# Optimization experiments

Measured on AMD Instinct MI355X. Metric: run time of the kernel, lower is better.

The kernel has to match this reference:

```python
import jax, jax.numpy as jnp
import numpy as np

S = 64            # rendered_size
CLASS_NUM = 14    # dataset.enc_len
NEG_SLOPE = 0.01
EPS = 1e-5


def _conv(x, w, stride, pad):
    return jax.lax.conv_general_dilated(
        x, w, (stride, stride), [(pad, pad), (pad, pad)],
        dimension_numbers=("NCHW", "OIHW", "NCHW"))


def _bn(x, gamma, beta):
    # BatchNorm2d in training mode: biased batch stats over (N,H,W)
    m = jnp.mean(x, axis=(0, 2, 3), keepdims=True)
    v = jnp.var(x, axis=(0, 2, 3), keepdims=True)
    xn = (x - m) * jax.lax.rsqrt(v + EPS)
    return xn * gamma.reshape(1, -1, 1, 1) + beta.reshape(1, -1, 1, 1)


def _lrelu(x):
    return jnp.where(x >= 0, x, NEG_SLOPE * x)


def _render(elements):
    # elements: (B, N, class_num+4)
    rects = elements[:, :, -4:]
    cls = elements[:, :, :-4]                       # (B, N, C)
    x = rects[:, :, 0][:, :, None, None] * S        # (B, N, 1, 1)
    y = rects[:, :, 1][:, :, None, None] * S
    w = rects[:, :, 2][:, :, None, None] * S
    h = rects[:, :, 3][:, :, None, None] * S
    x0, x1 = x - 0.5 * w, x + 0.5 * w
    y0, y1 = y - 0.5 * h, y + 0.5 * h
    cx = jnp.arange(S, dtype=elements.dtype)[None, None, None, :]  # varies along W
    cy = jnp.arange(S, dtype=elements.dtype)[None, None, :, None]  # varies along H
    k = lambda c, cr: jnp.maximum(1.0 - jnp.abs(c - cr), 0.0)
    b0 = lambda c, cr: jnp.clip(c - cr, 0.0, 1.0)
    b1 = lambda cr, c: jnp.clip(cr - c, 0.0, 1.0)
    by = b0(cy, y0) * b1(y1, cy)                    # (B, N, S, S)
    bx = b0(cx, x0) * b1(x1, cx)
    l0 = k(cx, x0) * by
    l1 = k(cx, x1) * by
    l2 = k(cy, y0) * bx
    l3 = k(cy, y1) * bx
    rendered = jnp.maximum(jnp.maximum(l0, l1), jnp.maximum(l2, l3))  # (B,N,S,S)
    # sum over elements of class one-hot * rendered -> (B, C, S, S)
    return jnp.einsum("bnc,bnhw->bchw", cls, rendered)


def setup_inputs() -> dict:
    key = jax.random.key(0)
    ks = jax.random.split(key, 8)
    B, N = 64, 46
    inp = {
        "input_data": jax.random.uniform(ks[0], (B, N, CLASS_NUM + 4), dtype=jnp.float32),
        "input_length": jax.random.randint(ks[1], (B,), 0, N, dtype=jnp.int32),
        # cnn convs (bias=False) + BN affine params
        "w1": jax.random.normal(ks[2], (64, CLASS_NUM, 5, 5), jnp.float32) * 0.05,
        "g1": jnp.ones((64,), jnp.float32), "b1": jnp.zeros((64,), jnp.float32),
        "w2": jax.random.normal(ks[3], (128, 64, 5, 5), jnp.float32) * 0.03,
        "g2": jnp.ones((128,), jnp.float32), "b2": jnp.zeros((128,), jnp.float32),
        "w3": jax.random.normal(ks[4], (256, 128, 5, 5), jnp.float32) * 0.02,
        "g3": jnp.ones((256,), jnp.float32), "b3": jnp.zeros((256,), jnp.float32),
        # classifier: conv k=8 (bias=False) + BN + 1x1 conv (bias=True)
        "w4": jax.random.normal(ks[5], (1024, 256, 8, 8), jnp.float32) * 0.01,
        "g4": jnp.ones((1024,), jnp.float32), "b4": jnp.zeros((1024,), jnp.float32),
        "w5": jax.random.normal(ks[6], (1, 1024, 1, 1), jnp.float32) * 0.03,
        "b5": jnp.zeros((1,), jnp.float32),
    }
    return inp


def reference(input_data, input_length, w1, g1, b1, w2, g2, b2,
              w3, g3, b3, w4, g4, b4, w5, b5):
    rendered = _render(input_data)                       # (B, C, 64, 64)
    h = _lrelu(_bn(_conv(rendered, w1, 2, 2), g1, b1))   # (B, 64, 32, 32)
    h = _lrelu(_bn(_conv(h, w2, 2, 2), g2, b2))          # (B, 128, 16, 16)
    h = _lrelu(_bn(_conv(h, w3, 2, 2), g3, b3))          # (B, 256, 8, 8)
    h = _lrelu(_bn(_conv(h, w4, 1, 0), g4, b4))          # (B, 1024, 1, 1)
    out = _conv(h, w5, 1, 0) + b5.reshape(1, -1, 1, 1)   # (B, 1, 1, 1)
    return out.squeeze()                                 # (B,)
```

## Files before the change

kernel.cpp:

```cpp
#include <hip/hip_runtime.h>
#include <hip/hip_bf16.h>

#define NEG 0.01f
#define EPS 1e-5f

typedef __attribute__((ext_vector_type(8))) short short8;
typedef __attribute__((ext_vector_type(4))) float floatx4;

__device__ inline unsigned short f2bf(float f) {
    __hip_bfloat16 h = __float2bfloat16(f);
    union { __hip_bfloat16 h; unsigned short u; } cv; cv.h = h;
    return cv.u;
}

__global__ __launch_bounds__(256) void render_kernel(const float* __restrict__ in,
                                                     unsigned short* __restrict__ out) {
    int b = blockIdx.x >> 4;
    int chunk = blockIdx.x & 15;
    __shared__ float r0[46], r1[46], r2[46], r3[46];
    __shared__ float cls_s[46 * 14];
    int tid = threadIdx.x;
    if (tid < 46) {
        const float* p = in + ((size_t)b * 46 + tid) * 18 + 14;
        float x = p[0] * 64.f, y = p[1] * 64.f, w = p[2] * 64.f, h = p[3] * 64.f;
        r0[tid] = x - 0.5f * w; r1[tid] = x + 0.5f * w;
        r2[tid] = y - 0.5f * h; r3[tid] = y + 0.5f * h;
    }
    for (int idx = tid; idx < 46 * 14; idx += 256) {
        int n = idx / 14, c = idx % 14;
        cls_s[idx] = in[((size_t)b * 46 + n) * 18 + c];
    }
    __syncthreads();
    if (tid < 33) {
        int j = chunk * 33 + tid;
        if (j < 528) {
            int y, x;
            if (j < 136) { y = j / 68; x = j - y * 68; }
            else if (j < 272) { int t = j - 136; int yy = t / 68; y = 66 + yy; x = t - yy * 68; }
            else { int t = j - 272; y = 2 + (t >> 2); int k = t & 3; x = (k < 2) ? k : 64 + k; }
            size_t zb = (((size_t)b * 68 + y) * 68 + x) * 16;
            short8 z;
#pragma unroll
            for (int i = 0; i < 8; ++i) z[i] = 0;
            *(short8*)(out + zb) = z;
            *(short8*)(out + zb + 8) = z;
        }
    }
    int pix = chunk * 256 + tid;
    float cx = (float)(pix & 63);
    float cy = (float)(pix >> 6);
    float acc[14];
#pragma unroll
    for (int c = 0; c < 14; ++c) acc[c] = 0.f;
    for (int n = 0; n < 46; ++n) {
        float x0 = r0[n], x1 = r1[n], y0 = r2[n], y1 = r3[n];
        float by = fminf(fmaxf(cy - y0, 0.f), 1.f) * fminf(fmaxf(y1 - cy, 0.f), 1.f);
        float bx = fminf(fmaxf(cx - x0, 0.f), 1.f) * fminf(fmaxf(x1 - cx, 0.f), 1.f);
        float kx0 = fmaxf(1.f - fabsf(cx - x0), 0.f);
        float kx1 = fmaxf(1.f - fabsf(cx - x1), 0.f);
        float ky0 = fmaxf(1.f - fabsf(cy - y0), 0.f);
        float ky1 = fmaxf(1.f - fabsf(cy - y1), 0.f);
        float r = fmaxf(fmaxf(kx0 * by, kx1 * by), fmaxf(ky0 * bx, ky1 * bx));
        if (r > 0.f) {
#pragma unroll
            for (int c = 0; c < 14; ++c) acc[c] = fmaf(cls_s[n * 14 + c], r, acc[c]);
        }
    }
    size_t obase = (((size_t)b * 68 + ((pix >> 6) + 2)) * 68 + ((pix & 63) + 2)) * 16;
    short8 v0, v1;
#pragma unroll
    for (int i = 0; i < 8; ++i) v0[i] = (short)f2bf(acc[i]);
#pragma unroll
    for (int i = 0; i < 6; ++i) v1[i] = (short)f2bf(acc[8 + i]);
    v1[6] = 0; v1[7] = 0;
    *(short8*)(out + obase) = v0;
    *(short8*)(out + obase + 8) = v1;
}

__global__ __launch_bounds__(256) void wtrans_all(const float* __restrict__ w1,
                                                  const float* __restrict__ w2,
                                                  const float* __restrict__ w3,
                                                  unsigned short* __restrict__ wT1,
                                                  unsigned short* __restrict__ wT2,
                                                  unsigned short* __restrict__ wT3) {
    int idx = blockIdx.x * 256 + threadIdx.x;
    const float* w; unsigned short* wT; int CIN, CPLOG, SUB, COLOG;
    if (idx < 30720) { w = w1; wT = wT1; CIN = 14; CPLOG = 4; SUB = 3; COLOG = 6; }
    else if (idx < 235520) { idx -= 30720; w = w2; wT = wT2; CIN = 64; CPLOG = 6; SUB = 10; COLOG = 7; }
    else if (idx < 1054720) { idx -= 235520; w = w3; wT = wT3; CIN = 128; CPLOG = 7; SUB = 20; COLOG = 8; }
    else return;
    int kk = idx & 31;
    int co = (idx >> 5) & ((1 << COLOG) - 1);
    int s = idx >> (5 + COLOG);
    int kh = s / SUB, sub = s - kh * SUB;
    int kidx = sub * 32 + kk;
    int kw = kidx >> CPLOG;
    int ci = kidx & ((1 << CPLOG) - 1);
    float v = (kw < 5 && ci < CIN) ? w[((size_t)(co * CIN + ci) * 5 + kh) * 5 + kw] : 0.f;
    wT[idx] = f2bf(v);
}

template <int CP, int COUT, int HP, int LOG_OHW, int LOG_OW, int SUB,
          int NCO, int NT, int CH, int NW>
__global__ __launch_bounds__(NW * 64) void conv_mfma(
        const unsigned short* __restrict__ inP,
        const unsigned short* __restrict__ wT,
        float* __restrict__ outX,
        float* __restrict__ stacc) {
    constexpr int NSTEP = 5 * SUB;
    constexpr int NCHUNK = NSTEP / CH;
    constexpr int COT = NT * 16;
    constexpr int NSTG = (CH * COT * 4) / (NW * 64);
    static_assert(NSTEP % CH == 0, "CH must divide NSTEP");
    static_assert((CH * COT * 4) % (NW * 64) == 0, "staging must tile evenly");
    __shared__ short Bs[2][CH][COT][32];
    __shared__ float sred[NW][2][COT];
    int tid = threadIdx.x;
    int wave = tid >> 6, lane = tid & 63, q = lane >> 4, l16 = lane & 15;
    int bm = blockIdx.x / NCO, bco = blockIdx.x % NCO;

    const short* aB[4];
#pragma unroll
    for (int f = 0; f < 4; ++f) {
        int m = bm * (NW * 64) + wave * 64 + f * 16 + l16;
        int b = m >> LOG_OHW;
        int ohw = m & ((1 << LOG_OHW) - 1);
        int oh = ohw >> LOG_OW, ow = ohw & ((1 << LOG_OW) - 1);
        aB[f] = (const short*)inP + ((size_t)((b * HP + 2 * oh) * HP + 2 * ow)) * CP + q * 8;
    }
    const short* bgbase = (const short*)wT + (size_t)bco * COT * 32;

    floatx4 acc[4][NT];
#pragma unroll
    for (int f = 0; f < 4; ++f)
#pragma unroll
        for (int nt = 0; nt < NT; ++nt) acc[f][nt] = (floatx4){0.f, 0.f, 0.f, 0.f};

    short8 nb[NSTG];
#pragma unroll
    for (int i = 0; i < NSTG; ++i) {
        int v = tid + i * NW * 64;
        int s = v / (COT * 4);
        int rem = v - s * (COT * 4);
        nb[i] = *(const short8*)(bgbase + ((size_t)s * COUT) * 32 + rem * 8);
    }
#pragma unroll
    for (int i = 0; i < NSTG; ++i) {
        int v = tid + i * NW * 64;
        int s = v / (COT * 4);
        int rem = v - s * (COT * 4);
        *(short8*)((short*)&Bs[0][s][0][0] + rem * 8) = nb[i];
    }
    __syncthreads();

    for (int chunk = 0; chunk < NCHUNK; ++chunk) {
        int cur = chunk & 1;
        if (chunk + 1 < NCHUNK) {
            int step0 = (chunk + 1) * CH;
#pragma unroll
            for (int i = 0; i < NSTG; ++i) {
                int v = tid + i * NW * 64;
                int s = v / (COT * 4);
                int rem = v - s * (COT * 4);
                nb[i] = *(const short8*)(bgbase + ((size_t)(step0 + s) * COUT) * 32 + rem * 8);
            }
        }
#pragma unroll
        for (int s = 0; s < CH; ++s) {
            int step = chunk * CH + s;
            int kh = step / SUB, sub = step - kh * SUB;
            short8 af[4];
#pragma unroll
            for (int f = 0; f < 4; ++f)
                af[f] = *(const short8*)(aB[f] + (size_t)(kh * HP) * CP + sub * 32);
#pragma unroll
            for (int nt = 0; nt < NT; ++nt) {
                short8 bf = *(const short8*)&Bs[cur][s][nt * 16 + l16][q * 8];
#pragma unroll
                for (int f = 0; f < 4; ++f)
                    acc[f][nt] = __builtin_amdgcn_mfma_f32_16x16x32_bf16(af[f], bf, acc[f][nt], 0, 0, 0);
            }
        }
        if (chunk + 1 < NCHUNK) {
#pragma unroll
            for (int i = 0; i < NSTG; ++i) {
                int v = tid + i * NW * 64;
                int s = v / (COT * 4);
                int rem = v - s * (COT * 4);
                *(short8*)((short*)&Bs[cur ^ 1][s][0][0] + rem * 8) = nb[i];
            }
            __syncthreads();
        }
    }
#pragma unroll
    for (int f = 0; f < 4; ++f)
#pragma unroll
        for (int nt = 0; nt < NT; ++nt)
#pragma unroll
            for (int rg = 0; rg < 4; ++rg) {
                int mg = bm * (NW * 64) + wave * 64 + f * 16 + q * 4 + rg;
                int co = bco * COT + nt * 16 + l16;
                outX[(size_t)mg * COUT + co] = acc[f][nt][rg];
            }
#pragma unroll
    for (int nt = 0; nt < NT; ++nt) {
        float s = 0.f, s2 = 0.f;
#pragma unroll
        for (int f = 0; f < 4; ++f)
#pragma unroll
            for (int rg = 0; rg < 4; ++rg) {
                float v = acc[f][nt][rg];
                s += v; s2 = fmaf(v, v, s2);
            }
        s += __shfl_xor(s, 16); s += __shfl_xor(s, 32);
        s2 += __shfl_xor(s2, 16); s2 += __shfl_xor(s2, 32);
        if (q == 0) {
            sred[wave][0][nt * 16 + l16] = s;
            sred[wave][1][nt * 16 + l16] = s2;
        }
    }
    __syncthreads();
    if (tid < COT) {
        float ts = 0.f, ts2 = 0.f;
#pragma unroll
        for (int w = 0; w < NW; ++w) { ts += sred[w][0][tid]; ts2 += sred[w][1][tid]; }
        atomicAdd(&stacc[bco * COT + tid], ts);
        atomicAdd(&stacc[COUT + bco * COT + tid], ts2);
    }
}

__global__ __launch_bounds__(256) void conv4_mfma(const unsigned short* __restrict__ A,
                                                  const float* __restrict__ w4,
                                                  float* __restrict__ h4) {
    constexpr int CH = 4, NCHUNK = 8;
    __shared__ short Bs[CH][64][40];
    int tid = threadIdx.x;
    int bco = blockIdx.x & 15;
    int ks = blockIdx.x >> 4;
    int wave = tid >> 6, lane = tid & 63, q = lane >> 4, l16 = lane & 15;
    const short* aBase = (const short*)A + (size_t)(wave * 16 + l16) * 16384 + ks * 1024 + q * 8;
    int r = tid >> 2, cc = tid & 3;
    const float* bg = w4 + (size_t)(bco * 64 + r) * 16384 + ks * 1024 + cc * 8;

    floatx4 acc[4];
#pragma unroll
    for (int nt = 0; nt < 4; ++nt) acc[nt] = (floatx4){0.f, 0.f, 0.f, 0.f};

    short8 nb[CH];
#pragma unroll
    for (int s = 0; s < CH; ++s) {
        float4 b0 = *(const float4*)(bg + s * 32);
        float4 b1 = *(const float4*)(bg + s * 32 + 4);
        nb[s][0] = (short)f2bf(b0.x); nb[s][1] = (short)f2bf(b0.y);
        nb[s][2] = (short)f2bf(b0.z); nb[s][3] = (short)f2bf(b0.w);
        nb[s][4] = (short)f2bf(b1.x); nb[s][5] = (short)f2bf(b1.y);
        nb[s][6] = (short)f2bf(b1.z); nb[s][7] = (short)f2bf(b1.w);
    }
#pragma unroll
    for (int s = 0; s < CH; ++s) *(short8*)&Bs[s][r][cc * 8] = nb[s];
    __syncthreads();

    for (int chunk = 0; chunk < NCHUNK; ++chunk) {
        bool has_next = (chunk + 1 < NCHUNK);
        if (has_next) {
#pragma unroll
            for (int s = 0; s < CH; ++s) {
                int step = (chunk + 1) * CH + s;
                float4 b0 = *(const float4*)(bg + step * 32);
                float4 b1 = *(const float4*)(bg + step * 32 + 4);
                nb[s][0] = (short)f2bf(b0.x); nb[s][1] = (short)f2bf(b0.y);
                nb[s][2] = (short)f2bf(b0.z); nb[s][3] = (short)f2bf(b0.w);
                nb[s][4] = (short)f2bf(b1.x); nb[s][5] = (short)f2bf(b1.y);
                nb[s][6] = (short)f2bf(b1.z); nb[s][7] = (short)f2bf(b1.w);
            }
        }
#pragma unroll
        for (int s = 0; s < CH; ++s) {
            int step = chunk * CH + s;
            short8 af = *(const short8*)(aBase + step * 32);
#pragma unroll
            for (int nt = 0; nt < 4; ++nt) {
                short8 bf = *(const short8*)&Bs[s][nt * 16 + l16][q * 8];
                acc[nt] = __builtin_amdgcn_mfma_f32_16x16x32_bf16(af, bf, acc[nt], 0, 0, 0);
            }
        }
        if (has_next) {
            __syncthreads();
#pragma unroll
            for (int s = 0; s < CH; ++s) *(short8*)&Bs[s][r][cc * 8] = nb[s];
            __syncthreads();
        }
    }
#pragma unroll
    for (int nt = 0; nt < 4; ++nt) {
#pragma unroll
        for (int rg = 0; rg < 4; ++rg) {
            int mg = wave * 16 + q * 4 + rg;
            int co = bco * 64 + nt * 16 + l16;
            atomicAdd(&h4[(size_t)mg * 1024 + co], acc[nt][rg]);
        }
    }
}

__global__ __launch_bounds__(256) void stats_part(const float* __restrict__ X,
                                                  float* __restrict__ acc,
                                                  int CO, int R, int RPB, int CGLOG) {
    int tid = threadIdx.x;
    int cg = blockIdx.x & ((1 << CGLOG) - 1);
    int rb = blockIdx.x >> CGLOG;
    int c = (cg << 6) + (tid & 63);
    int w = tid >> 6;
    float s = 0.f, s2 = 0.f;
    int rend = min(R, (rb + 1) * RPB);
    for (int r = rb * RPB + w; r < rend; r += 4) {
        float v = X[(size_t)r * CO + c];
        s += v; s2 += v * v;
    }
    __shared__ float ls[4][64], ls2[4][64];
    ls[w][tid & 63] = s; ls2[w][tid & 63] = s2;
    __syncthreads();
    if (tid < 64) {
        float ts = ls[0][tid] + ls[1][tid] + ls[2][tid] + ls[3][tid];
        float ts2 = ls2[0][tid] + ls2[1][tid] + ls2[2][tid] + ls2[3][tid];
        int cc = (cg << 6) + tid;
        atomicAdd(&acc[cc], ts);
        atomicAdd(&acc[CO + cc], ts2);
    }
}

__global__ __launch_bounds__(256) void bnpad_kernel(const float* __restrict__ X,
                                                    const float* __restrict__ stacc,
                                                    const float* __restrict__ g,
                                                    const float* __restrict__ bb,
                                                    unsigned short* __restrict__ out,
                                                    int CO_LOG, int OH, int OHP,
                                                    float invN, int total) {
    int idx = blockIdx.x * 256 + threadIdx.x;
    if (idx >= total) return;
    int CO = 1 << CO_LOG;
    int c = idx & (CO - 1);
    float mean = stacc[c] * invN;
    float var = fmaxf(stacc[CO + c] * invN - mean * mean, 0.f);
    float sc = g[c] * rsqrtf(var + EPS);
    float sh = bb[c] - mean * sc;
    int t = idx >> CO_LOG;
    int x = t % OHP; t /= OHP;
    int y = t % OHP; int b = t / OHP;
    unsigned short v = 0;
    if (y >= 2 && y < OH + 2 && x >= 2 && x < OH + 2) {
        float f = X[(((size_t)(b * OH + (y - 2)) * OH + (x - 2)) << CO_LOG) + c];
        f = f * sc + sh;
        f = f >= 0.f ? f : NEG * f;
        v = f2bf(f);
    }
    out[idx] = v;
}

__global__ __launch_bounds__(256) void bn_nchw_kernel(const float* __restrict__ X,
                                                      const float* __restrict__ stacc,
                                                      const float* __restrict__ g,
                                                      const float* __restrict__ bb,
                                                      unsigned short* __restrict__ out,
                                                      int total) {
    int idx = blockIdx.x * 256 + threadIdx.x;
    if (idx >= total) return;
    int hw = idx & 63;
    int ci = (idx >> 6) & 255;
    int b = idx >> 14;
    float mean = stacc[ci] * (1.f / 4096.f);
    float var = fmaxf(stacc[256 + ci] * (1.f / 4096.f) - mean * mean, 0.f);
    float sc = g[ci] * rsqrtf(var + EPS);
    float sh = bb[ci] - mean * sc;
    float f = X[((size_t)(b * 64 + hw)) * 256 + ci] * sc + sh;
    f = f >= 0.f ? f : NEG * f;
    out[idx] = f2bf(f);
}

__global__ __launch_bounds__(256) void conv5_kernel(const float* __restrict__ X,
                                                    const float* __restrict__ stacc,
                                                    const float* __restrict__ g,
                                                    const float* __restrict__ bb,
                                                    const float* __restrict__ w5,
                                                    const float* __restrict__ b5,
                                                    float* __restrict__ out) {
    int b = blockIdx.x, tid = threadIdx.x;
    float s = 0.f;
    for (int c = tid; c < 1024; c += 256) {
        float mean = stacc[c] * (1.f / 64.f);
        float var = fmaxf(stacc[1024 + c] * (1.f / 64.f) - mean * mean, 0.f);
        float sc = g[c] * rsqrtf(var + EPS);
        float sh = bb[c] - mean * sc;
        float f = X[(size_t)b * 1024 + c] * sc + sh;
        f = f >= 0.f ? f : NEG * f;
        s = fmaf(f, w5[c], s);
    }
#pragma unroll
    for (int off = 32; off > 0; off >>= 1) s += __shfl_down(s, off);
    __shared__ float ls[4];
    if ((tid & 63) == 0) ls[tid >> 6] = s;
    __syncthreads();
    if (tid == 0) out[b] = ls[0] + ls[1] + ls[2] + ls[3] + b5[0];
}

extern "C" void kernel_launch(void* const* d_in, const int* in_sizes, int n_in,
                              void* d_out, int out_size, void* d_ws, size_t ws_size,
                              hipStream_t stream) {
    (void)in_sizes; (void)n_in; (void)out_size; (void)ws_size;
    const float* input_data = (const float*)d_in[0];
    const float* w1 = (const float*)d_in[2];
    const float* g1 = (const float*)d_in[3];
    const float* b1 = (const float*)d_in[4];
    const float* w2 = (const float*)d_in[5];
    const float* g2 = (const float*)d_in[6];
    const float* b2 = (const float*)d_in[7];
    const float* w3 = (const float*)d_in[8];
    const float* g3 = (const float*)d_in[9];
    const float* b3 = (const float*)d_in[10];
    const float* w4 = (const float*)d_in[11];
    const float* g4 = (const float*)d_in[12];
    const float* b4 = (const float*)d_in[13];
    const float* w5 = (const float*)d_in[14];
    const float* b5 = (const float*)d_in[15];

    char* ws = (char*)d_ws;
    float* regA = (float*)ws;
    char* wsB = ws + 16777216;
    char* wsC = wsB + 10616832;
    char* wsD = wsC + 9469952;
    float* h4  = (float*)wsD;
    float* st1 = (float*)(wsD + 262144);
    float* st2 = (float*)(wsD + 262656);
    float* st3 = (float*)(wsD + 263680);
    float* st4 = (float*)(wsD + 265728);
    unsigned short* wT1 = (unsigned short*)(wsD + 274432);
    unsigned short* wT2 = (unsigned short*)(wsD + 335872);
    unsigned short* wT3 = (unsigned short*)(wsD + 745472);

    unsigned short* rendered = (unsigned short*)wsC;
    float* conv1out = regA;
    unsigned short* pad1 = (unsigned short*)wsB;
    float* conv2out = (float*)wsC;
    unsigned short* pad2 = (unsigned short*)wsB;
    float* conv3out = regA;
    unsigned short* a4 = (unsigned short*)wsC;

    hipMemsetAsync(wsD, 0, 273920, stream);
    wtrans_all<<<4120, 256, 0, stream>>>(w1, w2, w3, wT1, wT2, wT3);
    render_kernel<<<1024, 256, 0, stream>>>(input_data, rendered);

    conv_mfma<16, 64, 68, 10, 5, 3, 1, 4, 5, 4><<<256, 256, 0, stream>>>(rendered, wT1, conv1out, st1);
    bnpad_kernel<<<20736, 256, 0, stream>>>(conv1out, st1, g1, b1, pad1, 6, 32, 36, 1.f / 65536.f, 5308416);

    conv_mfma<64, 128, 36, 8, 4, 10, 4, 2, 10, 4><<<256, 256, 0, stream>>>(pad1, wT2, conv2out, st2);
    bnpad_kernel<<<12800, 256, 0, stream>>>(conv2out, st2, g2, b2, pad2, 7, 16, 20, 1.f / 16384.f, 3276800);

    conv_mfma<128, 256, 20, 6, 3, 20, 8, 2, 10, 2><<<256, 128, 0, stream>>>(pad2, wT3, conv3out, st3);
    bn_nchw_kernel<<<4096, 256, 0, stream>>>(conv3out, st3, g3, b3, a4, 1048576);

    conv4_mfma<<<256, 256, 0, stream>>>(a4, w4, h4);
    stats_part<<<16, 256, 0, stream>>>(h4, st4, 1024, 64, 64, 4);

    conv5_kernel<<<64, 256, 0, stream>>>(h4, st4, g4, b4, w5, b5, (float*)d_out);
}
```

Measured before the change: 278.9 us.

## Fuse whole network into one persistent kernel with grid barriers

Replaces the sequence of separate kernel launches (weight transform, render, three convs, BN/pad passes, conv4, stats, conv5) with a single 256-block persistent kernel that moves between phases through atomic-counter grid barriers. It also appears to add split-K for conv3 with partial output buffers, and vectorizes the BN/pad pass to 8 channels per thread. The aim is to remove launch gaps and tail effects between the many small kernels. The cost is that all phases are limited to 256 blocks, and there is spin-wait barrier overhead plus a co-residency assumption for correctness.

```diff
diff --git a/kernel.cpp b/kernel.cpp
--- a/kernel.cpp
+++ b/kernel.cpp
@@ -13,111 +13,40 @@
     return cv.u;
 }
 
-__global__ __launch_bounds__(256) void render_kernel(const float* __restrict__ in,
-                                                     unsigned short* __restrict__ out) {
-    int b = blockIdx.x >> 4;
-    int chunk = blockIdx.x & 15;
-    __shared__ float r0[46], r1[46], r2[46], r3[46];
-    __shared__ float cls_s[46 * 14];
-    int tid = threadIdx.x;
-    if (tid < 46) {
-        const float* p = in + ((size_t)b * 46 + tid) * 18 + 14;
-        float x = p[0] * 64.f, y = p[1] * 64.f, w = p[2] * 64.f, h = p[3] * 64.f;
-        r0[tid] = x - 0.5f * w; r1[tid] = x + 0.5f * w;
-        r2[tid] = y - 0.5f * h; r3[tid] = y + 0.5f * h;
-    }
-    for (int idx = tid; idx < 46 * 14; idx += 256) {
-        int n = idx / 14, c = idx % 14;
-        cls_s[idx] = in[((size_t)b * 46 + n) * 18 + c];
-    }
+__device__ __forceinline__ void gbar(unsigned* __restrict__ bar, int phase) {
     __syncthreads();
-    if (tid < 33) {
-        int j = chunk * 33 + tid;
-        if (j < 528) {
-            int y, x;
-            if (j < 136) { y = j / 68; x = j - y * 68; }
-            else if (j < 272) { int t = j - 136; int yy = t / 68; y = 66 + yy; x = t - yy * 68; }
-            else { int t = j - 272; y = 2 + (t >> 2); int k = t & 3; x = (k < 2) ? k : 64 + k; }
-            size_t zb = (((size_t)b * 68 + y) * 68 + x) * 16;
-            short8 z;
-#pragma unroll
-            for (int i = 0; i < 8; ++i) z[i] = 0;
-            *(short8*)(out + zb) = z;
-            *(short8*)(out + zb + 8) = z;
-        }
-    }
-    int pix = chunk * 256 + tid;
-    float cx = (float)(pix & 63);
-    float cy = (float)(pix >> 6);
-    float acc[14];
-#pragma unroll
-    for (int c = 0; c < 14; ++c) acc[c] = 0.f;
-    for (int n = 0; n < 46; ++n) {
-        float x0 = r0[n], x1 = r1[n], y0 = r2[n], y1 = r3[n];
-        float by = fminf(fmaxf(cy - y0, 0.f), 1.f) * fminf(fmaxf(y1 - cy, 0.f), 1.f);
-        float bx = fminf(fmaxf(cx - x0, 0.f), 1.f) * fminf(fmaxf(x1 - cx, 0.f), 1.f);
-        float kx0 = fmaxf(1.f - fabsf(cx - x0), 0.f);
-        float kx1 = fmaxf(1.f - fabsf(cx - x1), 0.f);
-        float ky0 = fmaxf(1.f - fabsf(cy - y0), 0.f);
-        float ky1 = fmaxf(1.f - fabsf(cy - y1), 0.f);
-        float r = fmaxf(fmaxf(kx0 * by, kx1 * by), fmaxf(ky0 * bx, ky1 * bx));
-        if (r > 0.f) {
-#pragma unroll
-            for (int c = 0; c < 14; ++c) acc[c] = fmaf(cls_s[n * 14 + c], r, acc[c]);
-        }
-    }
-    size_t obase = (((size_t)b * 68 + ((pix >> 6) + 2)) * 68 + ((pix & 63) + 2)) * 16;
-    short8 v0, v1;
-#pragma unroll
-    for (int i = 0; i < 8; ++i) v0[i] = (short)f2bf(acc[i]);
-#pragma unroll
-    for (int i = 0; i < 6; ++i) v1[i] = (short)f2bf(acc[8 + i]);
-    v1[6] = 0; v1[7] = 0;
-    *(short8*)(out + obase) = v0;
-    *(short8*)(out + obase + 8) = v1;
+    if (threadIdx.x == 0) {
+        __threadfence();
+        __hip_atomic_fetch_add(&bar[phase], 1u, __ATOMIC_RELEASE, __HIP_MEMORY_SCOPE_AGENT);
+        while (__hip_atomic_load(&bar[phase], __ATOMIC_ACQUIRE, __HIP_MEMORY_SCOPE_AGENT) < 256u)
+            __builtin_amdgcn_s_sleep(8);
+        __threadfence();
+    }
+    __syncthreads();
 }
 
-__global__ __launch_bounds__(256) void wtrans_all(const float* __restrict__ w1,
-                                                  const float* __restrict__ w2,
-                                                  const float* __restrict__ w3,
-                                                  unsigned short* __restrict__ wT1,
-                                                  unsigned short* __restrict__ wT2,
-                                                  unsigned short* __restrict__ wT3) {
-    int idx = blockIdx.x * 256 + threadIdx.x;
-    const float* w; unsigned short* wT; int CIN, CPLOG, SUB, COLOG;
-    if (idx < 30720) { w = w1; wT = wT1; CIN = 14; CPLOG = 4; SUB = 3; COLOG = 6; }
-    else if (idx < 235520) { idx -= 30720; w = w2; wT = wT2; CIN = 64; CPLOG = 6; SUB = 10; COLOG = 7; }
-    else if (idx < 1054720) { idx -= 235520; w = w3; wT = wT3; CIN = 128; CPLOG = 7; SUB = 20; COLOG = 8; }
-    else return;
-    int kk = idx & 31;
-    int co = (idx >> 5) & ((1 << COLOG) - 1);
-    int s = idx >> (5 + COLOG);
-    int kh = s / SUB, sub = s - kh * SUB;
-    int kidx = sub * 32 + kk;
-    int kw = kidx >> CPLOG;
-    int ci = kidx & ((1 << CPLOG) - 1);
-    float v = (kw < 5 && ci < CIN) ? w[((size_t)(co * CIN + ci) * 5 + kh) * 5 + kw] : 0.f;
-    wT[idx] = f2bf(v);
-}
-
 template <int CP, int COUT, int HP, int LOG_OHW, int LOG_OW, int SUB,
-          int NCO, int NT, int CH, int NW>
-__global__ __launch_bounds__(NW * 64) void conv_mfma(
+          int NCO, int NT, int CH, int NW, int KS, bool STATS>
+__device__ __forceinline__ void conv_phase(int bid, int tid,
         const unsigned short* __restrict__ inP,
         const unsigned short* __restrict__ wT,
-        float* __restrict__ outX,
-        float* __restrict__ stacc) {
+        float* __restrict__ out, float* __restrict__ stacc,
+        char* __restrict__ smemRaw) {
     constexpr int NSTEP = 5 * SUB;
-    constexpr int NCHUNK = NSTEP / CH;
+    constexpr int SSTEP = NSTEP / KS;
+    constexpr int NCHUNK = SSTEP / CH;
     constexpr int COT = NT * 16;
     constexpr int NSTG = (CH * COT * 4) / (NW * 64);
-    static_assert(NSTEP % CH == 0, "CH must divide NSTEP");
-    static_assert((CH * COT * 4) % (NW * 64) == 0, "staging must tile evenly");
-    __shared__ short Bs[2][CH][COT][32];
-    __shared__ float sred[NW][2][COT];
-    int tid = threadIdx.x;
+    constexpr int NM = 256 / (KS * NCO);
+    constexpr int M = NM * NW * 64;
+    typedef short (*BsT)[CH][COT][32];
+    BsT Bs = (BsT)smemRaw;
+    float* sred = (float*)(smemRaw + 2 * CH * COT * 32 * 2);
     int wave = tid >> 6, lane = tid & 63, q = lane >> 4, l16 = lane & 15;
-    int bm = blockIdx.x / NCO, bco = blockIdx.x % NCO;
+    int ks = bid / (NM * NCO);
+    int rem = bid - ks * (NM * NCO);
+    int bm = rem / NCO, bco = rem % NCO;
+    int sbase = ks * SSTEP;
 
     const short* aB[4];
 #pragma unroll
@@ -141,34 +70,34 @@
     for (int i = 0; i < NSTG; ++i) {
         int v = tid + i * NW * 64;
         int s = v / (COT * 4);
-        int rem = v - s * (COT * 4);
-        nb[i] = *(const short8*)(bgbase + ((size_t)s * COUT) * 32 + rem * 8);
+        int r2 = v - s * (COT * 4);
+        nb[i] = *(const short8*)(bgbase + ((size_t)(sbase + s) * COUT) * 32 + r2 * 8);
     }
 #pragma unroll
     for (int i = 0; i < NSTG; ++i) {
         int v = tid + i * NW * 64;
         int s = v / (COT * 4);
-        int rem = v - s * (COT * 4);
-        *(short8*)((short*)&Bs[0][s][0][0] + rem * 8) = nb[i];
+        int r2 = v - s * (COT * 4);
+        *(short8*)((short*)&Bs[0][s][0][0] + r2 * 8) = nb[i];
     }
     __syncthreads();
 
     for (int chunk = 0; chunk < NCHUNK; ++chunk) {
         int cur = chunk & 1;
         if (chunk + 1 < NCHUNK) {
-            int step0 = (chunk + 1) * CH;
+            int step0 = sbase + (chunk + 1) * CH;
 #pragma unroll
             for (int i = 0; i < NSTG; ++i) {
                 int v = tid + i * NW * 64;
                 int s = v / (COT * 4);
-                int rem = v - s * (COT * 4);
-                nb[i] = *(const short8*)(bgbase + ((size_t)(step0 + s) * COUT) * 32 + rem * 8);
+                int r2 = v - s * (COT * 4);
+                nb[i] = *(const short8*)(bgbase + ((size_t)(step0 + s) * COUT) * 32 + r2 * 8);
             }
         }
 #pragma unroll
         for (int s = 0; s < CH; ++s) {
-            int step = chunk * CH + s;
-            int kh = step / SUB, sub = step - kh * SUB;
+            int gstep = sbase + chunk * CH + s;
+            int kh = gstep / SUB, sub = gstep - kh * SUB;
             short8 af[4];
 #pragma unroll
             for (int f = 0; f < 4; ++f)
@@ -186,12 +115,13 @@
             for (int i = 0; i < NSTG; ++i) {
                 int v = tid + i * NW * 64;
                 int s = v / (COT * 4);
-                int rem = v - s * (COT * 4);
-                *(short8*)((short*)&Bs[cur ^ 1][s][0][0] + rem * 8) = nb[i];
+                int r2 = v - s * (COT * 4);
+                *(short8*)((short*)&Bs[cur ^ 1][s][0][0] + r2 * 8) = nb[i];
             }
             __syncthreads();
         }
     }
+    float* outK = out + (size_t)ks * M * COUT;
 #pragma unroll
     for (int f = 0; f < 4; ++f)
 #pragma unroll
@@ -200,206 +130,365 @@
             for (int rg = 0; rg < 4; ++rg) {
                 int mg = bm * (NW * 64) + wave * 64 + f * 16 + q * 4 + rg;
                 int co = bco * COT + nt * 16 + l16;
-                outX[(size_t)mg * COUT + co] = acc[f][nt][rg];
-            }
-#pragma unroll
-    for (int nt = 0; nt < NT; ++nt) {
+                outK[(size_t)mg * COUT + co] = acc[f][nt][rg];
+            }
+    if (STATS) {
+#pragma unroll
+        for (int nt = 0; nt < NT; ++nt) {
+            float s = 0.f, s2 = 0.f;
+#pragma unroll
+            for (int f = 0; f < 4; ++f)
+#pragma unroll
+                for (int rg = 0; rg < 4; ++rg) {
+                    float v = acc[f][nt][rg];
+                    s += v; s2 = fmaf(v, v, s2);
+                }
+            s += __shfl_xor(s, 16); s += __shfl_xor(s, 32);
+            s2 += __shfl_xor(s2, 16); s2 += __shfl_xor(s2, 32);
+            if (q == 0) {
+                sred[(wave * 2 + 0) * COT + nt * 16 + l16] = s;
+                sred[(wave * 2 + 1) * COT + nt * 16 + l16] = s2;
+            }
+        }
+        __syncthreads();
+        if (tid < COT) {
+            float ts = 0.f, ts2 = 0.f;
+#pragma unroll
+            for (int w = 0; w < NW; ++w) {
+                ts += sred[(w * 2 + 0) * COT + tid];
+                ts2 += sred[(w * 2 + 1) * COT + tid];
+            }
+            atomicAdd(&stacc[bco * COT + tid], ts);
+            atomicAdd(&stacc[COUT + bco * COT + tid], ts2);
+        }
+    }
+}
+
+template <int CO_LOG, int OH, int OHP, int ITERS>
+__device__ __forceinline__ void bnpad_phase(int bid, int tid,
+        const float* __restrict__ X, const float* __restrict__ stacc,
+        const float* __restrict__ g, const float* __restrict__ bb,
+        unsigned short* __restrict__ out, float invN, char* __restrict__ smemRaw) {
+    constexpr int CO = 1 << CO_LOG;
+    constexpr int TOTALV = 64 * OHP * OHP * (CO / 8);
+    float* sc_s = (float*)smemRaw;
+    float* sh_s = sc_s + CO;
+    if (tid < CO) {
+        float mean = stacc[tid] * invN;
+        float var = fmaxf(stacc[CO + tid] * invN - mean * mean, 0.f);
+        float sc = g[tid] * rsqrtf(var + EPS);
+        sc_s[tid] = sc;
+        sh_s[tid] = bb[tid] - mean * sc;
+    }
+    __syncthreads();
+    for (int i = 0; i < ITERS; ++i) {
+        int u = i * 65536 + (bid << 8) + tid;
+        if (u >= TOTALV) break;
+        int c0 = (u & (CO / 8 - 1)) << 3;
+        int t = u >> (CO_LOG - 3);
+        int x = t % OHP; t /= OHP;
+        int y = t % OHP; int b = t / OHP;
+        short8 sv;
+        if (y >= 2 && y < OH + 2 && x >= 2 && x < OH + 2) {
+            const float* src = X + (((size_t)((b * OH + (y - 2)) * OH + (x - 2))) << CO_LOG) + c0;
+            float4 a0 = *(const float4*)src;
+            float4 a1 = *(const float4*)(src + 4);
+            float vals[8] = {a0.x, a0.y, a0.z, a0.w, a1.x, a1.y, a1.z, a1.w};
+#pragma unroll
+            for (int j = 0; j < 8; ++j) {
+                float f = vals[j] * sc_s[c0 + j] + sh_s[c0 + j];
+                f = f >= 0.f ? f : NEG * f;
+                sv[j] = (short)f2bf(f);
+            }
+        } else {
+#pragma unroll
+            for (int j = 0; j < 8; ++j) sv[j] = 0;
+        }
+        *(short8*)(out + (size_t)u * 8) = sv;
+    }
+}
+
+__global__ __launch_bounds__(256) void mega_kernel(
+        const float* __restrict__ input_data,
+        const float* __restrict__ w1, const float* __restrict__ g1, const float* __restrict__ b1,
+        const float* __restrict__ w2, const float* __restrict__ g2, const float* __restrict__ b2,
+        const float* __restrict__ w3, const float* __restrict__ g3, const float* __restrict__ b3,
+        const float* __restrict__ w4, const float* __restrict__ g4, const float* __restrict__ b4,
+        const float* __restrict__ w5, const float* __restrict__ b5,
+        unsigned short* __restrict__ rendered,
+        float* __restrict__ conv1out, unsigned short* __restrict__ pad1,
+        float* __restrict__ conv2out, unsigned short* __restrict__ pad2,
+        float* __restrict__ conv3parts, unsigned short* __restrict__ a4,
+        float* __restrict__ h4,
+        float* __restrict__ st1, float* __restrict__ st2,
+        float* __restrict__ st3, float* __restrict__ st4,
+        unsigned short* __restrict__ wT1, unsigned short* __restrict__ wT2,
+        unsigned short* __restrict__ wT3,
+        unsigned* __restrict__ bar,
+        float* __restrict__ outF) {
+    __shared__ __align__(16) char smem[43008];
+    int tid = threadIdx.x;
+    int bid = blockIdx.x;
+
+    {
+        float* r0 = (float*)smem;
+        float* r1 = r0 + 46; float* r2 = r1 + 46; float* r3 = r2 + 46;
+        float* cls_s = r3 + 46;
+        for (int u = 0; u < 4; ++u) {
+            __syncthreads();
+            int rb = bid + u * 256;
+            int b = rb >> 4, chunk = rb & 15;
+            if (tid < 46) {
+                const float* p = input_data + ((size_t)b * 46 + tid) * 18 + 14;
+                float x = p[0] * 64.f, y = p[1] * 64.f, w = p[2] * 64.f, h = p[3] * 64.f;
+                r0[tid] = x - 0.5f * w; r1[tid] = x + 0.5f * w;
+                r2[tid] = y - 0.5f * h; r3[tid] = y + 0.5f * h;
+            }
+            for (int idx = tid; idx < 46 * 14; idx += 256) {
+                int n = idx / 14, c = idx % 14;
+                cls_s[idx] = input_data[((size_t)b * 46 + n) * 18 + c];
+            }
+            __syncthreads();
+            if (tid < 33) {
+                int j = chunk * 33 + tid;
+                if (j < 528) {
+                    int y, x;
+                    if (j < 136) { y = j / 68; x = j - y * 68; }
+                    else if (j < 272) { int t = j - 136; int yy = t / 68; y = 66 + yy; x = t - yy * 68; }
+                    else { int t = j - 272; y = 2 + (t >> 2); int k = t & 3; x = (k < 2) ? k : 64 + k; }
+                    size_t zb = (((size_t)b * 68 + y) * 68 + x) * 16;
+                    short8 z;
+#pragma unroll
+                    for (int i = 0; i < 8; ++i) z[i] = 0;
+                    *(short8*)(rendered + zb) = z;
+                    *(short8*)(rendered + zb + 8) = z;
+                }
+            }
+            int pix = chunk * 256 + tid;
+            float cx = (float)(pix & 63);
+            float cy = (float)(pix >> 6);
+            float acc[14];
+#pragma unroll
+            for (int c = 0; c < 14; ++c) acc[c] = 0.f;
+            for (int n = 0; n < 46; ++n) {
+                float x0 = r0[n], x1 = r1[n], y0 = r2[n], y1 = r3[n];
+                float by = fminf(fmaxf(cy - y0, 0.f), 1.f) * fminf(fmaxf(y1 - cy, 0.f), 1.f);
+                float bx = fminf(fmaxf(cx - x0, 0.f), 1.f) * fminf(fmaxf(x1 - cx, 0.f), 1.f);
+                float kx0 = fmaxf(1.f - fabsf(cx - x0), 0.f);
+                float kx1 = fmaxf(1.f - fabsf(cx - x1), 0.f);
+                float ky0 = fmaxf(1.f - fabsf(cy - y0), 0.f);
+                float ky1 = fmaxf(1.f - fabsf(cy - y1), 0.f);
+                float r = fmaxf(fmaxf(kx0 * by, kx1 * by), fmaxf(ky0 * bx, ky1 * bx));
+                if (r > 0.f) {
+#pragma unroll
+                    for (int c = 0; c < 14; ++c) acc[c] = fmaf(cls_s[n * 14 + c], r, acc[c]);
+                }
+            }
+            size_t ob = (((size_t)b * 68 + ((pix >> 6) + 2)) * 68 + ((pix & 63) + 2)) * 16;
+            short8 v0, v1;
+#pragma unroll
+            for (int i = 0; i < 8; ++i) v0[i] = (short)f2bf(acc[i]);
+#pragma unroll
+            for (int i = 0; i < 6; ++i) v1[i] = (short)f2bf(acc[8 + i]);
+            v1[6] = 0; v1[7] = 0;
+            *(short8*)(rendered + ob) = v0;
+            *(short8*)(rendered + ob + 8) = v1;
+        }
+        for (int i = 0; i < 17; ++i) {
+            int idx = i * 65536 + (bid << 8) + tid;
+            if (idx >= 1054720) break;
+            const float* w; unsigned short* wT; int CIN, CPLOG, SUB, COLOG;
+            if (idx < 30720) { w = w1; wT = wT1; CIN = 14; CPLOG = 4; SUB = 3; COLOG = 6; }
+            else if (idx < 235520) { idx -= 30720; w = w2; wT = wT2; CIN = 64; CPLOG = 6; SUB = 10; COLOG = 7; }
+            else { idx -= 235520; w = w3; wT = wT3; CIN = 128; CPLOG = 7; SUB = 20; COLOG = 8; }
+            int kk = idx & 31;
+            int co = (idx >> 5) & ((1 << COLOG) - 1);
+            int s = idx >> (5 + COLOG);
+            int kh = s / SUB, sub = s - kh * SUB;
+            int kidx = sub * 32 + kk;
+            int kw = kidx >> CPLOG;
+            int ci = kidx & ((1 << CPLOG) - 1);
+            float v = (kw < 5 && ci < CIN) ? w[((size_t)(co * CIN + ci) * 5 + kh) * 5 + kw] : 0.f;
+            wT[idx] = f2bf(v);
+        }
+    }
+    gbar(bar, 0);
+
+    conv_phase<16, 64, 68, 10, 5, 3, 1, 4, 5, 4, 1, true>(bid, tid, rendered, wT1, conv1out, st1, smem);
+    gbar(bar, 1);
+
+    bnpad_phase<6, 32, 36, 11>(bid, tid, conv1out, st1, g1, b1, pad1, 1.f / 65536.f, smem);
+    gbar(bar, 2);
+
+    conv_phase<64, 128, 36, 8, 4, 10, 4, 2, 10, 4, 1, true>(bid, tid, pad1, wT2, conv2out, st2, smem);
+    gbar(bar, 3);
+
+    bnpad_phase<7, 16, 20, 7>(bid, tid, conv2out, st2, g2, b2, pad2, 1.f / 16384.f, smem);
+    gbar(bar, 4);
+
+    conv_phase<128, 256, 20, 6, 3, 20, 8, 2, 10, 4, 2, false>(bid, tid, pad2, wT3, conv3parts, (float*)0, smem);
+    gbar(bar, 5);
+
+    {
+        float* ls = (float*)smem;
+        float* ls2 = ls + 256;
+        int cg = bid & 3, rb = bid >> 2;
+        int c = (cg << 6) + (tid & 63);
+        int w = tid >> 6;
         float s = 0.f, s2 = 0.f;
-#pragma unroll
-        for (int f = 0; f < 4; ++f)
+        for (int r = rb * 64 + w; r < rb * 64 + 64; r += 4) {
+            float v = conv3parts[(size_t)r * 256 + c] + conv3parts[1048576 + (size_t)r * 256 + c];
+            s += v; s2 += v * v;
+        }
+        ls[(w << 6) + (tid & 63)] = s;
+        ls2[(w << 6) + (tid & 63)] = s2;
+        __syncthreads();
+        if (tid < 64) {
+            float ts = ls[tid] + ls[64 + tid] + ls[128 + tid] + ls[192 + tid];
+            float ts2 = ls2[tid] + ls2[64 + tid] + ls2[128 + tid] + ls2[192 + tid];
+            atomicAdd(&st3[(cg << 6) + tid], ts);
+            atomicAdd(&st3[256 + (cg << 6) + tid], ts2);
+        }
+    }
+    gbar(bar, 6);
+
+    {
+        float* sc_s = (float*)smem;
+        float* sh_s = sc_s + 256;
+        {
+            float mean = st3[tid] * (1.f / 4096.f);
+            float var = fmaxf(st3[256 + tid] * (1.f / 4096.f) - mean * mean, 0.f);
+            float sc = g3[tid] * rsqrtf(var + EPS);
+            sc_s[tid] = sc;
+            sh_s[tid] = b3[tid] - mean * sc;
+        }
+        __syncthreads();
+        for (int i = 0; i < 16; ++i) {
+            int idx = i * 65536 + (bid << 8) + tid;
+            int hw = idx & 63;
+            int ci = (idx >> 6) & 255;
+            int b = idx >> 14;
+            size_t base = ((size_t)(b * 64 + hw)) * 256 + ci;
+            float f = conv3parts[base] + conv3parts[base + 1048576];
+            f = f * sc_s[ci] + sh_s[ci];
+            f = f >= 0.f ? f : NEG * f;
+            a4[idx] = f2bf(f);
+        }
+    }
+    gbar(bar, 7);
+
+    {
+        constexpr int CH = 4, NCHUNK = 8;
+        typedef short (*BsT)[64][40];
+        BsT Bs = (BsT)smem;
+        int bco = bid & 15;
+        int ks = bid >> 4;
+        int wave = tid >> 6, lane = tid & 63, q = lane >> 4, l16 = lane & 15;
+        const short* aBase = (const short*)a4 + (size_t)(wave * 16 + l16) * 16384 + ks * 1024 + q * 8;
+        int r = tid >> 2, cc = tid & 3;
+        const float* bg = w4 + (size_t)(bco * 64 + r) * 16384 + ks * 1024 + cc * 8;
+
+        floatx4 acc[4];
+#pragma unroll
+        for (int nt = 0; nt < 4; ++nt) acc[nt] = (floatx4){0.f, 0.f, 0.f, 0.f};
+
+        short8 nb[CH];
+#pragma unroll
+        for (int s = 0; s < CH; ++s) {
+            float4 b0 = *(const float4*)(bg + s * 32);
+            float4 b1 = *(const float4*)(bg + s * 32 + 4);
+            nb[s][0] = (short)f2bf(b0.x); nb[s][1] = (short)f2bf(b0.y);
+            nb[s][2] = (short)f2bf(b0.z); nb[s][3] = (short)f2bf(b0.w);
+            nb[s][4] = (short)f2bf(b1.x); nb[s][5] = (short)f2bf(b1.y);
+            nb[s][6] = (short)f2bf(b1.z); nb[s][7] = (short)f2bf(b1.w);
+        }
+#pragma unroll
+        for (int s = 0; s < CH; ++s) *(short8*)&Bs[s][r][cc * 8] = nb[s];
+        __syncthreads();
+
+        for (int chunk = 0; chunk < NCHUNK; ++chunk) {
+            bool has_next = (chunk + 1 < NCHUNK);
+            if (has_next) {
+#pragma unroll
+                for (int s = 0; s < CH; ++s) {
+                    int step = (chunk + 1) * CH + s;
+                    float4 b0 = *(const float4*)(bg + step * 32);
+                    float4 b1 = *(const float4*)(bg + step * 32 + 4);
+                    nb[s][0] = (short)f2bf(b0.x); nb[s][1] = (short)f2bf(b0.y);
+                    nb[s][2] = (short)f2bf(b0.z); nb[s][3] = (short)f2bf(b0.w);
+                    nb[s][4] = (short)f2bf(b1.x); nb[s][5] = (short)f2bf(b1.y);
+                    nb[s][6] = (short)f2bf(b1.z); nb[s][7] = (short)f2bf(b1.w);
+                }
+            }
+#pragma unroll
+            for (int s = 0; s < CH; ++s) {
+                int step = chunk * CH + s;
+                short8 af = *(const short8*)(aBase + step * 32);
+#pragma unroll
+                for (int nt = 0; nt < 4; ++nt) {
+                    short8 bf = *(const short8*)&Bs[s][nt * 16 + l16][q * 8];
+                    acc[nt] = __builtin_amdgcn_mfma_f32_16x16x32_bf16(af, bf, acc[nt], 0, 0, 0);
+                }
+            }
+            if (has_next) {
+                __syncthreads();
+#pragma unroll
+                for (int s = 0; s < CH; ++s) *(short8*)&Bs[s][r][cc * 8] = nb[s];
+                __syncthreads();
+            }
+        }
+#pragma unroll
+        for (int nt = 0; nt < 4; ++nt)
 #pragma unroll
             for (int rg = 0; rg < 4; ++rg) {
-                float v = acc[f][nt][rg];
-                s += v; s2 = fmaf(v, v, s2);
-            }
-        s += __shfl_xor(s, 16); s += __shfl_xor(s, 32);
-        s2 += __shfl_xor(s2, 16); s2 += __shfl_xor(s2, 32);
-        if (q == 0) {
-            sred[wave][0][nt * 16 + l16] = s;
-            sred[wave][1][nt * 16 + l16] = s2;
-        }
-    }
-    __syncthreads();
-    if (tid < COT) {
-        float ts = 0.f, ts2 = 0.f;
-#pragma unroll
-        for (int w = 0; w < NW; ++w) { ts += sred[w][0][tid]; ts2 += sred[w][1][tid]; }
-        atomicAdd(&stacc[bco * COT + tid], ts);
-        atomicAdd(&stacc[COUT + bco * COT + tid], ts2);
-    }
-}
-
-__global__ __launch_bounds__(256) void conv4_mfma(const unsigned short* __restrict__ A,
-                                                  const float* __restrict__ w4,
-                                                  float* __restrict__ h4) {
-    constexpr int CH = 4, NCHUNK = 8;
-    __shared__ short Bs[CH][64][40];
-    int tid = threadIdx.x;
-    int bco = blockIdx.x & 15;
-    int ks = blockIdx.x >> 4;
-    int wave = tid >> 6, lane = tid & 63, q = lane >> 4, l16 = lane & 15;
-    const short* aBase = (const short*)A + (size_t)(wave * 16 + l16) * 16384 + ks * 1024 + q * 8;
-    int r = tid >> 2, cc = tid & 3;
-    const float* bg = w4 + (size_t)(bco * 64 + r) * 16384 + ks * 1024 + cc * 8;
-
-    floatx4 acc[4];
-#pragma unroll
-    for (int nt = 0; nt < 4; ++nt) acc[nt] = (floatx4){0.f, 0.f, 0.f, 0.f};
-
-    short8 nb[CH];
-#pragma unroll
-    for (int s = 0; s < CH; ++s) {
-        float4 b0 = *(const float4*)(bg + s * 32);
-        float4 b1 = *(const float4*)(bg + s * 32 + 4);
-        nb[s][0] = (short)f2bf(b0.x); nb[s][1] = (short)f2bf(b0.y);
-        nb[s][2] = (short)f2bf(b0.z); nb[s][3] = (short)f2bf(b0.w);
-        nb[s][4] = (short)f2bf(b1.x); nb[s][5] = (short)f2bf(b1.y);
-        nb[s][6] = (short)f2bf(b1.z); nb[s][7] = (short)f2bf(b1.w);
-    }
-#pragma unroll
-    for (int s = 0; s < CH; ++s) *(short8*)&Bs[s][r][cc * 8] = nb[s];
-    __syncthreads();
-
-    for (int chunk = 0; chunk < NCHUNK; ++chunk) {
-        bool has_next = (chunk + 1 < NCHUNK);
-        if (has_next) {
-#pragma unroll
-            for (int s = 0; s < CH; ++s) {
-                int step = (chunk + 1) * CH + s;
-                float4 b0 = *(const float4*)(bg + step * 32);
-                float4 b1 = *(const float4*)(bg + step * 32 + 4);
-                nb[s][0] = (short)f2bf(b0.x); nb[s][1] = (short)f2bf(b0.y);
-                nb[s][2] = (short)f2bf(b0.z); nb[s][3] = (short)f2bf(b0.w);
-                nb[s][4] = (short)f2bf(b1.x); nb[s][5] = (short)f2bf(b1.y);
-                nb[s][6] = (short)f2bf(b1.z); nb[s][7] = (short)f2bf(b1.w);
-            }
-        }
-#pragma unroll
-        for (int s = 0; s < CH; ++s) {
-            int step = chunk * CH + s;
-            short8 af = *(const short8*)(aBase + step * 32);
-#pragma unroll
-            for (int nt = 0; nt < 4; ++nt) {
-                short8 bf = *(const short8*)&Bs[s][nt * 16 + l16][q * 8];
-                acc[nt] = __builtin_amdgcn_mfma_f32_16x16x32_bf16(af, bf, acc[nt], 0, 0, 0);
-            }
-        }
-        if (has_next) {
-            __syncthreads();
-#pragma unroll
-            for (int s = 0; s < CH; ++s) *(short8*)&Bs[s][r][cc * 8] = nb[s];
-            __syncthreads();
-        }
-    }
-#pragma unroll
-    for (int nt = 0; nt < 4; ++nt) {
-#pragma unroll
-        for (int rg = 0; rg < 4; ++rg) {
-            int mg = wave * 16 + q * 4 + rg;
-            int co = bco * 64 + nt * 16 + l16;
-            atomicAdd(&h4[(size_t)mg * 1024 + co], acc[nt][rg]);
-        }
-    }
-}
-
-__global__ __launch_bounds__(256) void stats_part(const float* __restrict__ X,
-                                                  float* __restrict__ acc,
-                                                  int CO, int R, int RPB, int CGLOG) {
-    int tid = threadIdx.x;
-    int cg = blockIdx.x & ((1 << CGLOG) - 1);
-    int rb = blockIdx.x >> CGLOG;
-    int c = (cg << 6) + (tid & 63);
-    int w = tid >> 6;
-    float s = 0.f, s2 = 0.f;
-    int rend = min(R, (rb + 1) * RPB);
-    for (int r = rb * RPB + w; r < rend; r += 4) {
-        float v = X[(size_t)r * CO + c];
-        s += v; s2 += v * v;
-    }
-    __shared__ float ls[4][64], ls2[4][64];
-    ls[w][tid & 63] = s; ls2[w][tid & 63] = s2;
-    __syncthreads();
-    if (tid < 64) {
-        float ts = ls[0][tid] + ls[1][tid] + ls[2][tid] + ls[3][tid];
-        float ts2 = ls2[0][tid] + ls2[1][tid] + ls2[2][tid] + ls2[3][tid];
-        int cc = (cg << 6) + tid;
-        atomicAdd(&acc[cc], ts);
-        atomicAdd(&acc[CO + cc], ts2);
-    }
-}
-
-__global__ __launch_bounds__(256) void bnpad_kernel(const float* __restrict__ X,
-                                                    const float* __restrict__ stacc,
-                                                    const float* __restrict__ g,
-                                                    const float* __restrict__ bb,
-                                                    unsigned short* __restrict__ out,
-                                                    int CO_LOG, int OH, int OHP,
-                                                    float invN, int total) {
-    int idx = blockIdx.x * 256 + threadIdx.x;
-    if (idx >= total) return;
-    int CO = 1 << CO_LOG;
-    int c = idx & (CO - 1);
-    float mean = stacc[c] * invN;
-    float var = fmaxf(stacc[CO + c] * invN - mean * mean, 0.f);
-    float sc = g[c] * rsqrtf(var + EPS);
-    float sh = bb[c] - mean * sc;
-    int t = idx >> CO_LOG;
-    int x = t % OHP; t /= OHP;
-    int y = t % OHP; int b = t / OHP;
-    unsigned short v = 0;
-    if (y >= 2 && y < OH + 2 && x >= 2 && x < OH + 2) {
-        float f = X[(((size_t)(b * OH + (y - 2)) * OH + (x - 2)) << CO_LOG) + c];
-        f = f * sc + sh;
-        f = f >= 0.f ? f : NEG * f;
-        v = f2bf(f);
-    }
-    out[idx] = v;
-}
-
-__global__ __launch_bounds__(256) void bn_nchw_kernel(const float* __restrict__ X,
-                                                      const float* __restrict__ stacc,
-                                                      const float* __restrict__ g,
-                                                      const float* __restrict__ bb,
-                                                      unsigned short* __restrict__ out,
-                                                      int total) {
-    int idx = blockIdx.x * 256 + threadIdx.x;
-    if (idx >= total) return;
-    int hw = idx & 63;
-    int ci = (idx >> 6) & 255;
-    int b = idx >> 14;
-    float mean = stacc[ci] * (1.f / 4096.f);
-    float var = fmaxf(stacc[256 + ci] * (1.f / 4096.f) - mean * mean, 0.f);
-    float sc = g[ci] * rsqrtf(var + EPS);
-    float sh = bb[ci] - mean * sc;
-    float f = X[((size_t)(b * 64 + hw)) * 256 + ci] * sc + sh;
-    f = f >= 0.f ? f : NEG * f;
-    out[idx] = f2bf(f);
-}
-
-__global__ __launch_bounds__(256) void conv5_kernel(const float* __restrict__ X,
-                                                    const float* __restrict__ stacc,
-                                                    const float* __restrict__ g,
-                                                    const float* __restrict__ bb,
-                                                    const float* __restrict__ w5,
-                                                    const float* __restrict__ b5,
-                                                    float* __restrict__ out) {
-    int b = blockIdx.x, tid = threadIdx.x;
-    float s = 0.f;
-    for (int c = tid; c < 1024; c += 256) {
-        float mean = stacc[c] * (1.f / 64.f);
-        float var = fmaxf(stacc[1024 + c] * (1.f / 64.f) - mean * mean, 0.f);
-        float sc = g[c] * rsqrtf(var + EPS);
-        float sh = bb[c] - mean * sc;
-        float f = X[(size_t)b * 1024 + c] * sc + sh;
-        f = f >= 0.f ? f : NEG * f;
-        s = fmaf(f, w5[c], s);
-    }
-#pragma unroll
-    for (int off = 32; off > 0; off >>= 1) s += __shfl_down(s, off);
-    __shared__ float ls[4];
-    if ((tid & 63) == 0) ls[tid >> 6] = s;
-    __syncthreads();
-    if (tid == 0) out[b] = ls[0] + ls[1] + ls[2] + ls[3] + b5[0];
+                int mg = wave * 16 + q * 4 + rg;
+                int co = bco * 64 + nt * 16 + l16;
+                atomicAdd(&h4[(size_t)mg * 1024 + co], acc[nt][rg]);
+            }
+    }
+    gbar(bar, 8);
+
+    if (bid < 16) {
+        float* ls = (float*)smem;
+        float* ls2 = ls + 256;
+        int c = (bid << 6) + (tid & 63);
+        int w = tid >> 6;
+        float s = 0.f, s2 = 0.f;
+        for (int r = w; r < 64; r += 4) {
+            float v = h4[(size_t)r * 1024 + c];
+            s += v; s2 += v * v;
+        }
+        ls[(w << 6) + (tid & 63)] = s;
+        ls2[(w << 6) + (tid & 63)] = s2;
+        __syncthreads();
+        if (tid < 64) {
+            float ts = ls[tid] + ls[64 + tid] + ls[128 + tid] + ls[192 + tid];
+            float ts2 = ls2[tid] + ls2[64 + tid] + ls2[128 + tid] + ls2[192 + tid];
+            atomicAdd(&st4[(bid << 6) + tid], ts);
+            atomicAdd(&st4[1024 + (bid << 6) + tid], ts2);
+        }
+    }
+    gbar(bar, 9);
+
+    if (bid < 64) {
+        int b = bid;
+        float s = 0.f;
+        for (int c = tid; c < 1024; c += 256) {
+            float mean = st4[c] * (1.f / 64.f);
+            float var = fmaxf(st4[1024 + c] * (1.f / 64.f) - mean * mean, 0.f);
+            float sc = g4[c] * rsqrtf(var + EPS);
+            float sh = b4[c] - mean * sc;
+            float f = h4[(size_t)b * 1024 + c] * sc + sh;
+            f = f >= 0.f ? f : NEG * f;
+            s = fmaf(f, w5[c], s);
+        }
+#pragma unroll
+        for (int off = 32; off > 0; off >>= 1) s += __shfl_down(s, off);
+        float* ls = (float*)smem;
+        if ((tid & 63) == 0) ls[tid >> 6] = s;
+        __syncthreads();
+        if (tid == 0) outF[b] = ls[0] + ls[1] + ls[2] + ls[3] + b5[0];
+    }
 }
 
 extern "C" void kernel_launch(void* const* d_in, const int* in_sizes, int n_in,
@@ -423,42 +512,27 @@
     const float* b5 = (const float*)d_in[15];
 
     char* ws = (char*)d_ws;
-    float* regA = (float*)ws;
-    char* wsB = ws + 16777216;
-    char* wsC = wsB + 10616832;
-    char* wsD = wsC + 9469952;
-    float* h4  = (float*)wsD;
-    float* st1 = (float*)(wsD + 262144);
-    float* st2 = (float*)(wsD + 262656);
-    float* st3 = (float*)(wsD + 263680);
-    float* st4 = (float*)(wsD + 265728);
-    unsigned short* wT1 = (unsigned short*)(wsD + 274432);
-    unsigned short* wT2 = (unsigned short*)(wsD + 335872);
-    unsigned short* wT3 = (unsigned short*)(wsD + 745472);
-
-    unsigned short* rendered = (unsigned short*)wsC;
-    float* conv1out = regA;
-    unsigned short* pad1 = (unsigned short*)wsB;
-    float* conv2out = (float*)wsC;
-    unsigned short* pad2 = (unsigned short*)wsB;
-    float* conv3out = regA;
-    unsigned short* a4 = (unsigned short*)wsC;
-
-    hipMemsetAsync(wsD, 0, 273920, stream);
-    wtrans_all<<<4120, 256, 0, stream>>>(w1, w2, w3, wT1, wT2, wT3);
-    render_kernel<<<1024, 256, 0, stream>>>(input_data, rendered);
-
-    conv_mfma<16, 64, 68, 10, 5, 3, 1, 4, 5, 4><<<256, 256, 0, stream>>>(rendered, wT1, conv1out, st1);
-    bnpad_kernel<<<20736, 256, 0, stream>>>(conv1out, st1, g1, b1, pad1, 6, 32, 36, 1.f / 65536.f, 5308416);
-
-    conv_mfma<64, 128, 36, 8, 4, 10, 4, 2, 10, 4><<<256, 256, 0, stream>>>(pad1, wT2, conv2out, st2);
-    bnpad_kernel<<<12800, 256, 0, stream>>>(conv2out, st2, g2, b2, pad2, 7, 16, 20, 1.f / 16384.f, 3276800);
-
-    conv_mfma<128, 256, 20, 6, 3, 20, 8, 2, 10, 2><<<256, 128, 0, stream>>>(pad2, wT3, conv3out, st3);
-    bn_nchw_kernel<<<4096, 256, 0, stream>>>(conv3out, st3, g3, b3, a4, 1048576);
-
-    conv4_mfma<<<256, 256, 0, stream>>>(a4, w4, h4);
-    stats_part<<<16, 256, 0, stream>>>(h4, st4, 1024, 64, 64, 4);
-
-    conv5_kernel<<<64, 256, 0, stream>>>(h4, st4, g4, b4, w5, b5, (float*)d_out);
+    unsigned short* rendered   = (unsigned short*)(ws + 0);
+    float*          conv1out   = (float*)(ws + 9469952);
+    unsigned short* pad1       = (unsigned short*)(ws + 26247168);
+    float*          conv2out   = (float*)(ws + 36864000);
+    unsigned short* pad2       = (unsigned short*)(ws + 45252608);
+    float*          conv3parts = (float*)(ws + 51806208);
+    unsigned short* a4         = (unsigned short*)(ws + 60194816);
+    float*          h4         = (float*)(ws + 62291968);
+    float*          st1        = (float*)(ws + 62554112);
+    float*          st2        = (float*)(ws + 62554624);
+    float*          st3        = (float*)(ws + 62555648);
+    float*          st4        = (float*)(ws + 62557696);
+    unsigned*       bar        = (unsigned*)(ws + 62565888);
+    unsigned short* wT1        = (unsigned short*)(ws + 62566144);
+    unsigned short* wT2        = (unsigned short*)(ws + 62627584);
+    unsigned short* wT3        = (unsigned short*)(ws + 63037184);
+
+    hipMemsetAsync(ws + 62291968, 0, 274176, stream);
+
+    mega_kernel<<<256, 256, 0, stream>>>(
+        input_data, w1, g1, b1, w2, g2, b2, w3, g3, b3, w4, g4, b4, w5, b5,
+        rendered, conv1out, pad1, conv2out, pad2, conv3parts, a4, h4,
+        st1, st2, st3, st4, wT1, wT2, wT3, bar, (float*)d_out);
 }
```

After: 607.3 us. 2.18x slower.
